# Kernel tuning notes

Hardware: AMD Instinct MI355X
Metric: run time of the kernel (lower is better)

Reference implementation:

```python
import jax, jax.numpy as jnp
import numpy as np
import math

FACTOR = 5  # args.factor


def setup_inputs() -> dict:
    key = jax.random.key(0)
    kq, kk, kv, ki = jax.random.split(key, 4)
    B, L, H, D = 8, 2048, 8, 64
    sample_k = min(FACTOR * int(np.ceil(np.log(L))), L)  # 40
    return {
        "queries": jax.random.normal(kq, (B, L, H, D), dtype=jnp.float32),
        "keys": jax.random.normal(kk, (B, L, H, D), dtype=jnp.float32),
        "values": jax.random.normal(kv, (B, L, H, D), dtype=jnp.float32),
        "index_sample": jax.random.randint(ki, (L, sample_k), 0, L),
    }


def reference(queries, keys, values, index_sample):
    B, L_Q, H, D = queries.shape
    L_K = keys.shape[1]
    # [B, L, H, D] -> [B, H, L, D]
    Q = queries.transpose(0, 2, 1, 3)
    K = keys.transpose(0, 2, 1, 3)
    V = values.transpose(0, 2, 1, 3)

    u = min(FACTOR * int(np.ceil(np.log(L_Q))), L_Q)  # n_top

    # ---- _prob_QK: sampled scores + sparsity measure + top-u queries ----
    # gather sampled keys per query position: [B, H, L_Q, sample_k, D]
    K_sample = K[:, :, index_sample, :]
    Q_K_sample = jnp.einsum('bhqd,bhqsd->bhqs', Q, K_sample)  # [B,H,L_Q,S]
    M = Q_K_sample.max(-1) - Q_K_sample.mean(-1)              # [B,H,L_Q]
    _, M_top = jax.lax.top_k(M, u)                            # [B,H,u]

    Q_reduce = jnp.take_along_axis(Q, M_top[..., None], axis=2)  # [B,H,u,D]
    scores = jnp.einsum('bhud,bhkd->bhuk', Q_reduce, K) * (1.0 / math.sqrt(D))

    # ---- initial context: mean of V broadcast over queries ----
    context = jnp.broadcast_to(V.mean(axis=2, keepdims=True), (B, H, L_Q, D))

    # ---- update context at selected query positions ----
    attn = jax.nn.softmax(scores, axis=-1)                  # [B,H,u,L_K]
    ctx_upd = jnp.einsum('bhuk,bhkd->bhud', attn, V)        # [B,H,u,D]
    bi = jnp.arange(B)[:, None, None]
    hi = jnp.arange(H)[None, :, None]
    context = context.at[bi, hi, M_top].set(ctx_upd)

    # [B,H,L_Q,D] -> [B,L_Q,H*D]
    return context.transpose(0, 2, 1, 3).reshape(B, L_Q, H * D)
```

## Files before the change

### kernel.cpp

```cpp
#include <hip/hip_runtime.h>
#include <hip/hip_bf16.h>

#define BB 8
#define LL 2048
#define HH 8
#define DD 64
#define HD 512
#define SK 40
#define UU 40
#define NCHUNK 16
#define CHUNK 128

typedef float v4f __attribute__((ext_vector_type(4)));

static const size_t OFF_M     = 0;
static const size_t OFF_TOP   = 512ull * 1024;
static const size_t OFF_VPART = 592ull * 1024;
static const size_t OFF_MPART = 768ull * 1024;
static const size_t OFF_SPART = 960ull * 1024;
static const size_t OFF_OPART = 1152ull * 1024;

template <int CTRL>
__device__ __forceinline__ float dpp_add(float x) {
    int yi = __builtin_amdgcn_mov_dpp(__float_as_int(x), CTRL, 0xF, 0xF, true);
    return x + __int_as_float(yi);
}

__global__ __launch_bounds__(128, 4) void kA_sample_scores(
    const float* __restrict__ Q, const float* __restrict__ K,
    const int* __restrict__ IS, float* __restrict__ M)
{
    int blk = blockIdx.x;
    int b = blk & 7;
    int q = blk >> 3;
    int tid = threadIdx.x;
    int h = tid >> 4;
    int lane = tid & 15;

    const int* __restrict__ isq = IS + q * SK;
    size_t base = (size_t)b * LL * HD;
    int off = h * DD + lane * 4;
    v4f qv = __builtin_nontemporal_load(
        (const v4f*)(Q + base + (size_t)q * HD + off));
    const float* __restrict__ Kb = K + base;

    int sidx[SK];
#pragma unroll
    for (int s = 0; s < SK; ++s)
        sidx[s] = __builtin_amdgcn_readfirstlane(isq[s]);

    float mx = -1e30f, sm = 0.f;

#define KA_DOT(kv) { \
        float p = qv.x * kv.x + qv.y * kv.y + qv.z * kv.z + qv.w * kv.w; \
        p = dpp_add<0xB1>(p);     \
        p = dpp_add<0x4E>(p);     \
        p = dpp_add<0x141>(p);    \
        p = dpp_add<0x140>(p);    \
        mx = fmaxf(mx, p); \
        sm += p; }

#pragma unroll
    for (int bt = 0; bt < 5; ++bt) {
        const int sb = bt * 8;
        v4f k0 = *(const v4f*)(Kb + (size_t)sidx[sb + 0] * HD + off);
        v4f k1 = *(const v4f*)(Kb + (size_t)sidx[sb + 1] * HD + off);
        v4f k2 = *(const v4f*)(Kb + (size_t)sidx[sb + 2] * HD + off);
        v4f k3 = *(const v4f*)(Kb + (size_t)sidx[sb + 3] * HD + off);
        v4f k4 = *(const v4f*)(Kb + (size_t)sidx[sb + 4] * HD + off);
        v4f k5 = *(const v4f*)(Kb + (size_t)sidx[sb + 5] * HD + off);
        v4f k6 = *(const v4f*)(Kb + (size_t)sidx[sb + 6] * HD + off);
        v4f k7 = *(const v4f*)(Kb + (size_t)sidx[sb + 7] * HD + off);
        asm volatile("" : "+v"(k0), "+v"(k1), "+v"(k2), "+v"(k3),
                          "+v"(k4), "+v"(k5), "+v"(k6), "+v"(k7));
        KA_DOT(k0) KA_DOT(k1) KA_DOT(k2) KA_DOT(k3)
        KA_DOT(k4) KA_DOT(k5) KA_DOT(k6) KA_DOT(k7)
    }
#undef KA_DOT

    if (lane == 0)
        M[((size_t)(b * HH + h)) * LL + q] = mx - sm * (1.0f / SK);
}

__global__ __launch_bounds__(256) void kB_topk(
    const float* __restrict__ M, int* __restrict__ TopIdx)
{
    int bh = blockIdx.x;
    int tid = threadIdx.x;
    __shared__ unsigned keys[LL];
    __shared__ int      hist[4096];
    __shared__ int      sscan[256];
    __shared__ unsigned ckeyA[2048];
    __shared__ int      cidxA[2048];
    __shared__ unsigned ckeyB[2048];
    __shared__ int      cidxB[2048];
    __shared__ int ctr[8];

    const float* __restrict__ m = M + (size_t)bh * LL;
    for (int i = tid; i < 4096; i += 256) hist[i] = 0;
    if (tid < 8) ctr[tid] = 0;
    __syncthreads();

    for (int i = tid; i < LL; i += 256) {
        unsigned u = __float_as_uint(m[i]);
        u = (u & 0x80000000u) ? ~u : (u | 0x80000000u);
        keys[i] = u;
        atomicAdd(&hist[u >> 20], 1);
    }
    __syncthreads();
    {
        int p = 0;
#pragma unroll
        for (int j = 0; j < 16; ++j) p += hist[tid * 16 + j];
        sscan[tid] = p;
        __syncthreads();
        for (int o = 1; o < 256; o <<= 1) {
            int v = (tid + o < 256) ? sscan[tid + o] : 0;
            __syncthreads();
            sscan[tid] += v;
            __syncthreads();
        }
        int snext = (tid < 255) ? sscan[tid + 1] : 0;
        if (sscan[tid] >= UU && snext < UU) {
            int cum = snext;
            for (int bkt = tid * 16 + 15; bkt >= tid * 16; --bkt) {
                int c = hist[bkt];
                if (cum + c >= UU) { ctr[3] = bkt; ctr[4] = UU - cum; break; }
                cum += c;
            }
        }
    }
    __syncthreads();
    unsigned T1 = (unsigned)ctr[3];
    int k1 = ctr[4];
    for (int i = tid; i < LL; i += 256) {
        unsigned u = keys[i];
        unsigned bkt = u >> 20;
        if (bkt > T1) {
            int p = atomicAdd(&ctr[0], 1);
            TopIdx[bh * UU + p] = i;
        } else if (bkt == T1) {
            int p = atomicAdd(&ctr[1], 1);
            ckeyA[p] = u; cidxA[p] = i;
        }
    }
    __syncthreads();
    int nA = ctr[1];

    for (int i = tid; i < 4096; i += 256) hist[i] = 0;
    __syncthreads();
    for (int i = tid; i < nA; i += 256)
        atomicAdd(&hist[(ckeyA[i] >> 8) & 0xFFF], 1);
    __syncthreads();
    {
        int p = 0;
#pragma unroll
        for (int j = 0; j < 16; ++j) p += hist[tid * 16 + j];
        sscan[tid] = p;
        __syncthreads();
        for (int o = 1; o < 256; o <<= 1) {
            int v = (tid + o < 256) ? sscan[tid + o] : 0;
            __syncthreads();
            sscan[tid] += v;
            __syncthreads();
        }
        int snext = (tid < 255) ? sscan[tid + 1] : 0;
        if (sscan[tid] >= k1 && snext < k1) {
            int cum = snext;
            for (int bkt = tid * 16 + 15; bkt >= tid * 16; --bkt) {
                int c = hist[bkt];
                if (cum + c >= k1) { ctr[3] = bkt; ctr[4] = k1 - cum; break; }
                cum += c;
            }
        }
    }
    __syncthreads();
    unsigned T2 = (unsigned)ctr[3];
    int k2 = ctr[4];
    for (int i = tid; i < nA; i += 256) {
        unsigned u = ckeyA[i];
        unsigned bkt = (u >> 8) & 0xFFF;
        if (bkt > T2) {
            int p = atomicAdd(&ctr[0], 1);
            TopIdx[bh * UU + p] = cidxA[i];
        } else if (bkt == T2) {
            int p = atomicAdd(&ctr[2], 1);
            ckeyB[p] = u; cidxB[p] = cidxA[i];
        }
    }
    __syncthreads();
    int nB = ctr[2];

    for (int i = tid; i < 256; i += 256) hist[i] = 0;
    __syncthreads();
    for (int i = tid; i < nB; i += 256)
        atomicAdd(&hist[ckeyB[i] & 0xFF], 1);
    __syncthreads();
    {
        sscan[tid] = hist[tid];
        __syncthreads();
        for (int o = 1; o < 256; o <<= 1) {
            int v = (tid + o < 256) ? sscan[tid + o] : 0;
            __syncthreads();
            sscan[tid] += v;
            __syncthreads();
        }
        int snext = (tid < 255) ? sscan[tid + 1] : 0;
        if (sscan[tid] >= k2 && snext < k2) { ctr[3] = tid; ctr[4] = k2 - snext; }
    }
    __syncthreads();
    unsigned T3 = (unsigned)ctr[3];
    int k3 = ctr[4];
    for (int i = tid; i < nB; i += 256) {
        unsigned u = ckeyB[i];
        unsigned bkt = u & 0xFF;
        if (bkt > T3) {
            int p = atomicAdd(&ctr[0], 1);
            TopIdx[bh * UU + p] = cidxB[i];
        } else if (bkt == T3) {
            int p = atomicAdd(&ctr[5], 1);
            cidxA[p] = cidxB[i];
        }
    }
    __syncthreads();
    if (tid == 0) {
        int n = ctr[5];
        int basep = ctr[0];
        for (int r = 0; r < k3; ++r) {
            int bi = 1 << 30, bp = -1;
            for (int j = 0; j < n; ++j) {
                int id = cidxA[j];
                if (id >= 0 && id < bi) { bi = id; bp = j; }
            }
            TopIdx[bh * UU + basep + r] = bi;
            cidxA[bp] = -1;
        }
    }
}

__global__ __launch_bounds__(256) void kC_vmean(
    const float* __restrict__ V, float* __restrict__ Vpart)
{
    int bh = blockIdx.x >> 3;
    int ch = blockIdx.x & 7;
    int b = bh >> 3, h = bh & 7;
    int tid = threadIdx.x;
    int dq = tid & 15;
    int lg = tid >> 4;

    float4 acc = make_float4(0.f, 0.f, 0.f, 0.f);
    size_t base = ((size_t)b * LL + ch * 256) * HD + h * DD + dq * 4;
    for (int l = lg; l < 256; l += 16) {
        float4 v = *(const float4*)(V + base + (size_t)l * HD);
        acc.x += v.x; acc.y += v.y; acc.z += v.z; acc.w += v.w;
    }
    __shared__ float4 red[256];
    red[tid] = acc;
    __syncthreads();
    if (tid < 16) {
        float4 s = make_float4(0.f, 0.f, 0.f, 0.f);
#pragma unroll
        for (int g = 0; g < 16; ++g) {
            float4 v = red[g * 16 + tid];
            s.x += v.x; s.y += v.y; s.z += v.z; s.w += v.w;
        }
        *(float4*)(Vpart + ch * 4096 + bh * 64 + tid * 4) = s;
    }
}

__global__ __launch_bounds__(256) void kD_fill(
    const float* __restrict__ Vpart, float* __restrict__ out)
{
    size_t i4 = (size_t)blockIdx.x * 256 + threadIdx.x;
    size_t o = i4 * 4;
    int hd = (int)(o & (HD - 1));
    int b  = (int)(o >> 20);
    int h  = hd >> 6;
    int idx = (b * HH + h) * DD + (hd & 63);
    float4 acc = make_float4(0.f, 0.f, 0.f, 0.f);
#pragma unroll
    for (int c = 0; c < 8; ++c) {
        float4 v = *(const float4*)(Vpart + c * 4096 + idx);
        acc.x += v.x; acc.y += v.y; acc.z += v.z; acc.w += v.w;
    }
    const float sc = 1.0f / LL;
    float4 r; r.x = acc.x * sc; r.y = acc.y * sc; r.z = acc.z * sc; r.w = acc.w * sc;
    *(float4*)(out + o) = r;
}

__global__ __launch_bounds__(256, 4) void kE_attn_partial(
    const float* __restrict__ Q, const float* __restrict__ K, const float* __restrict__ V,
    const int* __restrict__ TopIdx,
    float* __restrict__ Opart, float* __restrict__ mpart, float* __restrict__ spart)
{
    int c  = blockIdx.x;
    int bh = blockIdx.y;
    int b = bh >> 3, h = bh & 7;
    int tid = threadIdx.x;

    __shared__ float Qs[UU * DD];
    __shared__ float PT[UU][CHUNK + 4];
    __shared__ int   qidx[UU];
    __shared__ float mred[UU], sred[UU];

    if (tid < UU) qidx[tid] = TopIdx[bh * UU + tid];
    __syncthreads();

    size_t hbase  = (size_t)b * LL * HD + h * DD;
    size_t kcbase = hbase + (size_t)c * CHUNK * HD;

    for (int r = tid; r < UU * 16; r += 256) {
        int u = r >> 4, j = r & 15;
        *(float4*)(Qs + u * DD + j * 4) =
            *(const float4*)(Q + hbase + (size_t)qidx[u] * HD + j * 4);
    }
    __syncthreads();

    {
        int w = tid >> 6;
        int lane = tid & 63;
        const float* __restrict__ K0 = K + kcbase + (size_t)lane * HD;
        const float* __restrict__ K1 = K0 + (size_t)64 * HD;

        float d0[10], d1[10];
#pragma unroll
        for (int i = 0; i < 10; ++i) { d0[i] = 0.f; d1[i] = 0.f; }

#pragma unroll 1
        for (int qt = 0; qt < 4; ++qt) {
            float4 ka[4], kb[4];
#pragma unroll
            for (int j = 0; j < 4; ++j) {
                ka[j] = *(const float4*)(K0 + qt * 16 + j * 4);
                kb[j] = *(const float4*)(K1 + qt * 16 + j * 4);
            }
#pragma unroll
            for (int j = 0; j < 4; ++j) {
#pragma unroll
                for (int uu = 0; uu < 10; ++uu) {
                    float4 qv = *(const float4*)(Qs + (w * 10 + uu) * DD + qt * 16 + j * 4);
                    d0[uu] += qv.x * ka[j].x + qv.y * ka[j].y + qv.z * ka[j].z + qv.w * ka[j].w;
                    d1[uu] += qv.x * kb[j].x + qv.y * kb[j].y + qv.z * kb[j].z + qv.w * kb[j].w;
                }
            }
        }

#pragma unroll
        for (int uu = 0; uu < 10; ++uu) {
            int u = w * 10 + uu;
            float x0 = d0[uu] * 0.125f;
            float x1 = d1[uu] * 0.125f;
            float m = fmaxf(x0, x1);
            m = fmaxf(m, __shfl_xor(m, 1));
            m = fmaxf(m, __shfl_xor(m, 2));
            m = fmaxf(m, __shfl_xor(m, 4));
            m = fmaxf(m, __shfl_xor(m, 8));
            m = fmaxf(m, __shfl_xor(m, 16));
            m = fmaxf(m, __shfl_xor(m, 32));
            float p0 = __expf(x0 - m);
            float p1 = __expf(x1 - m);
            PT[u][lane]      = p0;
            PT[u][lane + 64] = p1;
            float s = p0 + p1;
            s += __shfl_xor(s, 1);
            s += __shfl_xor(s, 2);
            s += __shfl_xor(s, 4);
            s += __shfl_xor(s, 8);
            s += __shfl_xor(s, 16);
            s += __shfl_xor(s, 32);
            if (lane == 0) { mred[u] = m; sred[u] = s; }
        }
    }
    __syncthreads();

    {
        int dq = tid & 15, ug4 = tid >> 4;
        float4 acc[3];
#pragma unroll
        for (int i = 0; i < 3; ++i) acc[i] = make_float4(0.f, 0.f, 0.f, 0.f);
        const float* __restrict__ Vb = V + kcbase + dq * 4;
        for (int l0 = 0; l0 < CHUNK; l0 += 8) {
            float4 v[8];
#pragma unroll
            for (int j = 0; j < 8; ++j)
                v[j] = *(const float4*)(Vb + (size_t)(l0 + j) * HD);
#pragma unroll
            for (int i = 0; i < 3; ++i) {
                int u = ug4 + 16 * i;
                if (u < UU) {
                    float4 pa = *(const float4*)(&PT[u][l0]);
                    float4 pb = *(const float4*)(&PT[u][l0 + 4]);
                    acc[i].x += pa.x * v[0].x + pa.y * v[1].x + pa.z * v[2].x + pa.w * v[3].x
                              + pb.x * v[4].x + pb.y * v[5].x + pb.z * v[6].x + pb.w * v[7].x;
                    acc[i].y += pa.x * v[0].y + pa.y * v[1].y + pa.z * v[2].y + pa.w * v[3].y
                              + pb.x * v[4].y + pb.y * v[5].y + pb.z * v[6].y + pb.w * v[7].y;
                    acc[i].z += pa.x * v[0].z + pa.y * v[1].z + pa.z * v[2].z + pa.w * v[3].z
                              + pb.x * v[4].z + pb.y * v[5].z + pb.z * v[6].z + pb.w * v[7].z;
                    acc[i].w += pa.x * v[0].w + pa.y * v[1].w + pa.z * v[2].w + pa.w * v[3].w
                              + pb.x * v[4].w + pb.y * v[5].w + pb.z * v[6].w + pb.w * v[7].w;
                }
            }
        }
#pragma unroll
        for (int i = 0; i < 3; ++i) {
            int u = ug4 + 16 * i;
            if (u < UU) {
                size_t ob = (((size_t)(bh * UU + u)) * NCHUNK + c) * DD + dq * 4;
                *(float4*)(Opart + ob) = acc[i];
            }
        }
    }
    if (tid < UU) {
        mpart[(bh * UU + tid) * NCHUNK + c] = mred[tid];
        spart[(bh * UU + tid) * NCHUNK + c] = sred[tid];
    }
}

__global__ __launch_bounds__(64) void kF_combine(
    const float* __restrict__ Opart, const float* __restrict__ mpart,
    const float* __restrict__ spart, const int* __restrict__ TopIdx,
    float* __restrict__ out)
{
    int g = blockIdx.x;
    int bh = g / UU;
    int b = bh >> 3, h = bh & 7;
    int d = threadIdx.x;

    float m_i[NCHUNK];
    float Mx = -1e30f;
#pragma unroll
    for (int i = 0; i < NCHUNK; ++i) { m_i[i] = mpart[g * NCHUNK + i]; Mx = fmaxf(Mx, m_i[i]); }
    float S = 0.f, O = 0.f;
#pragma unroll
    for (int i = 0; i < NCHUNK; ++i) {
        float w = __expf(m_i[i] - Mx);
        S += w * spart[g * NCHUNK + i];
        O += w * Opart[((size_t)g * NCHUNK + i) * DD + d];
    }
    int qi = TopIdx[g];
    out[((size_t)b * LL + qi) * HD + h * DD + d] = O / S;
}

extern "C" void kernel_launch(void* const* d_in, const int* in_sizes, int n_in,
                              void* d_out, int out_size, void* d_ws, size_t ws_size,
                              hipStream_t stream) {
    const float* Q  = (const float*)d_in[0];
    const float* K  = (const float*)d_in[1];
    const float* V  = (const float*)d_in[2];
    const int*   IS = (const int*)d_in[3];
    float* out = (float*)d_out;
    char* ws = (char*)d_ws;

    float* M      = (float*)(ws + OFF_M);
    int*   TopIdx = (int*)(ws + OFF_TOP);
    float* Vpart  = (float*)(ws + OFF_VPART);
    float* mpart  = (float*)(ws + OFF_MPART);
    float* spart  = (float*)(ws + OFF_SPART);
    float* Opart  = (float*)(ws + OFF_OPART);

    kA_sample_scores<<<BB * LL, 128, 0, stream>>>(Q, K, IS, M);
    kC_vmean<<<BB * HH * 8, 256, 0, stream>>>(V, Vpart);
    kB_topk<<<BB * HH, 256, 0, stream>>>(M, TopIdx);
    kD_fill<<<(BB * LL * HD) / (256 * 4), 256, 0, stream>>>(Vpart, out);
    kE_attn_partial<<<dim3(NCHUNK, BB * HH), 256, 0, stream>>>(Q, K, V, TopIdx,
                                                               Opart, mpart, spart);
    kF_combine<<<BB * HH * UU, 64, 0, stream>>>(Opart, mpart, spart, TopIdx, out);
}
```

Before: 247.2 us.

## Fuse V mean reduction into attention partial kernel and reorder block mapping

Drops the separate V-mean kernel. The attention-partial kernel now also sums each V chunk it already loads, writing per-chunk partial sums that the fill kernel reduces over 16 chunks. This removes a full extra pass over V and one launch. The grid is flattened with batch in the low bits, which changes block scheduling and locality. Fill now has to run after the attention kernel, and the workspace offsets are resized for the larger Vpart buffer.

```diff
diff --git a/kernel.cpp b/kernel.cpp
--- a/kernel.cpp
+++ b/kernel.cpp
@@ -15,9 +15,9 @@
 
 static const size_t OFF_M     = 0;
 static const size_t OFF_TOP   = 512ull * 1024;
-static const size_t OFF_VPART = 592ull * 1024;
-static const size_t OFF_MPART = 768ull * 1024;
-static const size_t OFF_SPART = 960ull * 1024;
+static const size_t OFF_VPART = 528ull * 1024;
+static const size_t OFF_MPART = 784ull * 1024;
+static const size_t OFF_SPART = 944ull * 1024;
 static const size_t OFF_OPART = 1152ull * 1024;
 
 template <int CTRL>
@@ -238,36 +238,6 @@
     }
 }
 
-__global__ __launch_bounds__(256) void kC_vmean(
-    const float* __restrict__ V, float* __restrict__ Vpart)
-{
-    int bh = blockIdx.x >> 3;
-    int ch = blockIdx.x & 7;
-    int b = bh >> 3, h = bh & 7;
-    int tid = threadIdx.x;
-    int dq = tid & 15;
-    int lg = tid >> 4;
-
-    float4 acc = make_float4(0.f, 0.f, 0.f, 0.f);
-    size_t base = ((size_t)b * LL + ch * 256) * HD + h * DD + dq * 4;
-    for (int l = lg; l < 256; l += 16) {
-        float4 v = *(const float4*)(V + base + (size_t)l * HD);
-        acc.x += v.x; acc.y += v.y; acc.z += v.z; acc.w += v.w;
-    }
-    __shared__ float4 red[256];
-    red[tid] = acc;
-    __syncthreads();
-    if (tid < 16) {
-        float4 s = make_float4(0.f, 0.f, 0.f, 0.f);
-#pragma unroll
-        for (int g = 0; g < 16; ++g) {
-            float4 v = red[g * 16 + tid];
-            s.x += v.x; s.y += v.y; s.z += v.z; s.w += v.w;
-        }
-        *(float4*)(Vpart + ch * 4096 + bh * 64 + tid * 4) = s;
-    }
-}
-
 __global__ __launch_bounds__(256) void kD_fill(
     const float* __restrict__ Vpart, float* __restrict__ out)
 {
@@ -279,7 +249,7 @@
     int idx = (b * HH + h) * DD + (hd & 63);
     float4 acc = make_float4(0.f, 0.f, 0.f, 0.f);
 #pragma unroll
-    for (int c = 0; c < 8; ++c) {
+    for (int c = 0; c < NCHUNK; ++c) {
         float4 v = *(const float4*)(Vpart + c * 4096 + idx);
         acc.x += v.x; acc.y += v.y; acc.z += v.z; acc.w += v.w;
     }
@@ -291,15 +261,20 @@
 __global__ __launch_bounds__(256, 4) void kE_attn_partial(
     const float* __restrict__ Q, const float* __restrict__ K, const float* __restrict__ V,
     const int* __restrict__ TopIdx,
-    float* __restrict__ Opart, float* __restrict__ mpart, float* __restrict__ spart)
+    float* __restrict__ Opart, float* __restrict__ mpart, float* __restrict__ spart,
+    float* __restrict__ Vpart)
 {
-    int c  = blockIdx.x;
-    int bh = blockIdx.y;
-    int b = bh >> 3, h = bh & 7;
+    int bid = blockIdx.x;
+    int b = bid & 7;
+    int r9 = bid >> 3;
+    int c = r9 & 15;
+    int h = r9 >> 4;
+    int bh = b * HH + h;
     int tid = threadIdx.x;
 
     __shared__ float Qs[UU * DD];
     __shared__ float PT[UU][CHUNK + 4];
+    __shared__ float vred[16][DD];
     __shared__ int   qidx[UU];
     __shared__ float mred[UU], sred[UU];
 
@@ -378,12 +353,20 @@
         float4 acc[3];
 #pragma unroll
         for (int i = 0; i < 3; ++i) acc[i] = make_float4(0.f, 0.f, 0.f, 0.f);
+        float4 vsum = make_float4(0.f, 0.f, 0.f, 0.f);
         const float* __restrict__ Vb = V + kcbase + dq * 4;
         for (int l0 = 0; l0 < CHUNK; l0 += 8) {
             float4 v[8];
 #pragma unroll
             for (int j = 0; j < 8; ++j)
                 v[j] = *(const float4*)(Vb + (size_t)(l0 + j) * HD);
+            if (ug4 == (l0 >> 3)) {
+#pragma unroll
+                for (int j = 0; j < 8; ++j) {
+                    vsum.x += v[j].x; vsum.y += v[j].y;
+                    vsum.z += v[j].z; vsum.w += v[j].w;
+                }
+            }
 #pragma unroll
             for (int i = 0; i < 3; ++i) {
                 int u = ug4 + 16 * i;
@@ -409,6 +392,15 @@
                 *(float4*)(Opart + ob) = acc[i];
             }
         }
+        *(float4*)(&vred[ug4][dq * 4]) = vsum;
+    }
+    __syncthreads();
+
+    if (tid < DD) {
+        float s = 0.f;
+#pragma unroll
+        for (int g = 0; g < 16; ++g) s += vred[g][tid];
+        Vpart[c * 4096 + bh * DD + tid] = s;
     }
     if (tid < UU) {
         mpart[(bh * UU + tid) * NCHUNK + c] = mred[tid];
@@ -459,10 +451,9 @@
     float* Opart  = (float*)(ws + OFF_OPART);
 
     kA_sample_scores<<<BB * LL, 128, 0, stream>>>(Q, K, IS, M);
-    kC_vmean<<<BB * HH * 8, 256, 0, stream>>>(V, Vpart);
     kB_topk<<<BB * HH, 256, 0, stream>>>(M, TopIdx);
+    kE_attn_partial<<<BB * HH * NCHUNK, 256, 0, stream>>>(Q, K, V, TopIdx,
+                                                          Opart, mpart, spart, Vpart);
     kD_fill<<<(BB * LL * HD) / (256 * 4), 256, 0, stream>>>(Vpart, out);
-    kE_attn_partial<<<dim3(NCHUNK, BB * HH), 256, 0, stream>>>(Q, K, V, TopIdx,
-                                                               Opart, mpart, spart);
     kF_combine<<<BB * HH * UU, 64, 0, stream>>>(Opart, mpart, spart, TopIdx, out);
 }
```

After: 248.1 us. Within noise of the previous version (+0.3%).
